# Performance work log

Measured on AMD Instinct MI355X. Metric: run time of the kernel, lower is better.

The kernel has to match this reference:

```python
import jax, jax.numpy as jnp
import numpy as np

B, L, N_IN, N_STATE = 32, 4096, 8, 8
C_IN, C_OUT = N_IN + N_STATE, N_STATE
H, M, N_LAYERS = 64, 64, 4


def setup_inputs() -> dict:
    key = jax.random.key(0)
    ks = jax.random.split(key, 16)
    s = 0.02
    return {
        "u": jax.random.normal(ks[0], (B, L, N_IN), jnp.float32),
        "z": jax.random.normal(ks[1], (B, N_STATE), jnp.float32),
        "t": jax.random.uniform(ks[2], (B, 1), jnp.float32),
        "w_lift": jax.random.normal(ks[3], (H, C_IN), jnp.float32) * s,
        "b_lift": jnp.zeros((H,), jnp.float32),
        "spec_wr": jax.random.normal(ks[4], (N_LAYERS, H, H, M), jnp.float32) / (H),
        "spec_wi": jax.random.normal(ks[5], (N_LAYERS, H, H, M), jnp.float32) / (H),
        "w_skip": jax.random.normal(ks[6], (N_LAYERS, H, H), jnp.float32) * s,
        "b_skip": jnp.zeros((N_LAYERS, H), jnp.float32),
        "w_p1": jax.random.normal(ks[7], (2 * H, H), jnp.float32) * s,
        "b_p1": jnp.zeros((2 * H,), jnp.float32),
        "w_p2": jax.random.normal(ks[8], (C_OUT, 2 * H), jnp.float32) * s,
        "b_p2": jnp.zeros((C_OUT,), jnp.float32),
    }


def _fno_forward(u, z, w_lift, b_lift, spec_wr, spec_wi, w_skip, b_skip, w_p1, b_p1, w_p2, b_p2):
    b, l, _ = u.shape
    rep_z = jnp.broadcast_to(z[:, None, :], (b, l, z.shape[1]))
    x = jnp.concatenate([u, rep_z], axis=-1)          # [B, L, C_in]
    x = jnp.transpose(x, (0, 2, 1))                   # [B, C_in, L]
    # lifting (1x1 conv)
    x = jnp.einsum("bcl,hc->bhl", x, w_lift) + b_lift[None, :, None]
    n_layers, _, _, m = spec_wr.shape
    for i in range(n_layers):
        xf = jnp.fft.rfft(x, axis=-1)                 # [B, H, L//2+1] complex
        w = spec_wr[i] + 1j * spec_wi[i]              # [H, H, M]
        of = jnp.einsum("bim,oim->bom", xf[..., :m], w)
        of = jnp.pad(of, ((0, 0), (0, 0), (0, xf.shape[-1] - m)))
        xs = jnp.fft.irfft(of, n=l, axis=-1)          # [B, H, L]
        sk = jnp.einsum("bil,oi->bol", x, w_skip[i]) + b_skip[i][None, :, None]
        x = xs + sk
        if i < n_layers - 1:
            x = jax.nn.gelu(x)
    # projection: H -> 2H -> C_out (1x1 convs)
    x = jax.nn.gelu(jnp.einsum("bhl,ph->bpl", x, w_p1) + b_p1[None, :, None])
    x = jnp.einsum("bpl,op->bol", x, w_p2) + b_p2[None, :, None]
    outs = jnp.transpose(x, (0, 2, 1))                # [B, L, C_out]
    return outs[:, -1, :]                             # [B, C_out]


def reference(u, z, t, w_lift, b_lift, spec_wr, spec_wi, w_skip, b_skip, w_p1, b_p1, w_p2, b_p2):
    # t is accepted by the original forward but unused in FNOProjection
    return _fno_forward(u, z, w_lift, b_lift, spec_wr, spec_wi, w_skip, b_skip, w_p1, b_p1, w_p2, b_p2)
```

## Files before the change

### kernel.cpp

```cpp
#include <hip/hip_runtime.h>
#include <math.h>

typedef _Float16 f16;
typedef f16  f16x2 __attribute__((ext_vector_type(2)));
typedef f16  f16x4 __attribute__((ext_vector_type(4)));
typedef f16  f16x8 __attribute__((ext_vector_type(8)));
typedef float f32x4 __attribute__((ext_vector_type(4)));

#define F4(p)  (*(float4*)(p))
#define CF4(p) (*(const float4*)(p))

namespace {
constexpr int LL = 4096;
constexpr int HH = 64;
constexpr int NCH = 16;

__device__ __forceinline__ float gelu_fast(float x) {
    float inner = 0.7978845608028654f * (x + 0.044715f * x * x * x);
    float e = __expf(-2.0f * inner);
    return x / (1.0f + e);
}

__device__ __forceinline__ f32x4 mfma16(f16x8 a, f16x8 b, f32x4 c) {
    return __builtin_amdgcn_mfma_f32_16x16x32_f16(a, b, c, 0, 0, 0);
}
}

__global__ __launch_bounds__(256) void k_init(const float* __restrict__ u,
                                              const float* __restrict__ z,
                                              const float* __restrict__ wl,
                                              const float* __restrict__ bl,
                                              const float* __restrict__ wsk,
                                              const float* __restrict__ wr,
                                              const float* __restrict__ wi,
                                              f16* __restrict__ Tdt,
                                              f16* __restrict__ Ttr,
                                              f16* __restrict__ wskh,
                                              f16* __restrict__ wrh,
                                              f16* __restrict__ wih,
                                              f16* __restrict__ XT0) {
    const int bid = blockIdx.x;
    const int t = threadIdx.x;
    if (bid < 512) {
        const int b = bid >> 4;
        const int l0 = (bid & 15) * 256;
        constexpr int IP = 260;
        __shared__ float in_s[16 * IP];
        __shared__ float wsh[64 * 16];
        __shared__ float bsh[64];
        for (int i = t; i < 1024; i += 256) wsh[i] = wl[i];
        if (t < 64) bsh[t] = bl[t];
#pragma unroll
        for (int q = 0; q < 2; ++q) {
            int f = t + q * 256;
            int l = f >> 1, cq = (f & 1) * 4;
            float4 v = CF4(u + ((size_t)b * LL + l0 + l) * 8 + cq);
            in_s[(cq + 0) * IP + l] = v.x;
            in_s[(cq + 1) * IP + l] = v.y;
            in_s[(cq + 2) * IP + l] = v.z;
            in_s[(cq + 3) * IP + l] = v.w;
        }
        for (int f = t; f < 8 * 256; f += 256) {
            int c = f >> 8, l = f & 255;
            in_s[(8 + c) * IP + l] = z[b * 8 + c];
        }
        __syncthreads();
        const int hg = t >> 5, lsub = t & 31;
        float acc[8][8] = {};
        for (int c = 0; c < 16; ++c) {
            float wv[8], inv[8];
#pragma unroll
            for (int i = 0; i < 8; ++i) wv[i] = wsh[(hg * 8 + i) * 16 + c];
#pragma unroll
            for (int j = 0; j < 8; ++j) inv[j] = in_s[c * IP + lsub + 32 * j];
#pragma unroll
            for (int i = 0; i < 8; ++i)
#pragma unroll
                for (int j = 0; j < 8; ++j) acc[i][j] += wv[i] * inv[j];
        }
#pragma unroll
        for (int j = 0; j < 8; ++j) {
            __attribute__((aligned(16))) f16 hv[8];
#pragma unroll
            for (int i = 0; i < 8; ++i) hv[i] = (f16)(acc[i][j] + bsh[hg * 8 + i]);
            int l = l0 + lsub + 32 * j;
            F4(XT0 + ((size_t)b * LL + l) * HH + hg * 8) = CF4(hv);
        }
    } else if (bid < 1536) {
        const int tb = bid - 512;
        const float w0 = 6.283185307179586f / 4096.0f;
        {
            int m = tb >> 4;
            int l = ((tb & 15) << 8) + t;
            float s, c;
            sincosf((float)((l * m) & 4095) * w0, &s, &c);
            Tdt[(size_t)(2 * m) * LL + l]     = (f16)c;
            Tdt[(size_t)(2 * m + 1) * LL + l] = (f16)(-s);
        }
        {
            int l = tb * 4 + (t >> 6);
            int m = t & 63;
            float s, c;
            sincosf((float)((l * m) & 4095) * w0, &s, &c);
            const float sc = 1.0f / 4096.0f;
            f16x2 pv;
            pv.x = (f16)((m == 0) ? sc : 2.0f * sc * c);
            pv.y = (f16)((m == 0) ? 0.0f : -2.0f * sc * s);
            *(f16x2*)(Ttr + (size_t)l * 128 + 2 * m) = pv;
        }
        if (tb < 64) {
            int idx = tb * 256 + t;
            wskh[idx] = (f16)wsk[idx];
        }
    } else {
        const int cb = bid - 1536;
        size_t base = (size_t)cb * 1024 + t * 4;
        float4 vr = CF4(wr + base);
        float4 vi = CF4(wi + base);
        f16x4 hr, hi;
        hr.x = (f16)vr.x; hr.y = (f16)vr.y; hr.z = (f16)vr.z; hr.w = (f16)vr.w;
        hi.x = (f16)vi.x; hi.y = (f16)vi.y; hi.z = (f16)vi.z; hi.w = (f16)vi.w;
        *(f16x4*)(wrh + base) = hr;
        *(f16x4*)(wih + base) = hi;
    }
}

__global__ __launch_bounds__(256) void k_dft(const f16* __restrict__ XT,
                                             const f16* __restrict__ Tdt,
                                             f16* __restrict__ Y) {
    __shared__ f16 Asl[32 * 72];
    __shared__ f16 Bsl[128 * 72];
    const int t = threadIdx.x;
    const int ch = blockIdx.x >> 1, h0 = (blockIdx.x & 1) * 32, b = blockIdx.y;
    const int lane = t & 63, wid = t >> 6;
    const int mh = (wid & 1) * 16, n0 = (wid >> 1) * 64;
    const int fm = lane & 15, fq = lane >> 4;
    const int seg = t >> 6;
    const int br = t >> 3, bcol = (t & 7) * 8;
    f32x4 acc[4] = {};
    f16x8 rA;
    float4 rb[4];
    auto ldAB = [&](int k0) {
        const int l0 = ch * 256 + k0;
        rA = *(const f16x8*)(XT + ((size_t)b * LL + l0 + lane) * HH + h0 + seg * 8);
#pragma unroll
        for (int p = 0; p < 4; ++p)
            rb[p] = CF4(Tdt + (size_t)(br + p * 32) * LL + l0 + bcol);
    };
    auto wrAB = [&]() {
#pragma unroll
        for (int i = 0; i < 8; ++i) Asl[(seg * 8 + i) * 72 + lane] = rA[i];
#pragma unroll
        for (int p = 0; p < 4; ++p)
            F4(&Bsl[(br + p * 32) * 72 + bcol]) = rb[p];
    };
    ldAB(0);
    wrAB();
    for (int k0 = 0; k0 < 256; k0 += 64) {
        if (k0 < 192) ldAB(k0 + 64);
        __syncthreads();
#pragma unroll
        for (int ks = 0; ks < 64; ks += 32) {
            f16x8 a = *(const f16x8*)&Asl[(mh + fm) * 72 + ks + fq * 8];
#pragma unroll
            for (int j = 0; j < 4; ++j) {
                f16x8 bj = *(const f16x8*)&Bsl[(n0 + j * 16 + fm) * 72 + ks + fq * 8];
                acc[j] = mfma16(a, bj, acc[j]);
            }
        }
        __syncthreads();
        if (k0 < 192) wrAB();
    }
    f16* yp = Y + ((size_t)ch * 2048 + b * HH + h0) * 128;
#pragma unroll
    for (int j = 0; j < 4; ++j)
#pragma unroll
        for (int r = 0; r < 4; ++r)
            yp[(size_t)(mh + fq * 4 + r) * 128 + n0 + j * 16 + fm] = (f16)acc[j][r];
}

__global__ __launch_bounds__(256) void k_spec(const f16* __restrict__ Y,
                                              const f16* __restrict__ wrh,
                                              const f16* __restrict__ wih,
                                              f16* __restrict__ Ofh, int layer) {
    __shared__ float xsh[64 * 128];
    const int t = threadIdx.x;
    const int b = blockIdx.x;
    const int og = blockIdx.y;
    {
#pragma unroll
        for (int i = 0; i < 4; ++i) {
            int g = t + i * 256;
            float s[8] = {};
#pragma unroll
            for (int c = 0; c < NCH; ++c) {
                f16x8 v = *(const f16x8*)(Y + ((size_t)c * 2048 + b * HH) * 128 + g * 8);
#pragma unroll
                for (int e = 0; e < 8; ++e) s[e] += (float)v[e];
            }
#pragma unroll
            for (int e = 0; e < 8; ++e) xsh[g * 8 + e] = s[e];
        }
    }
    __syncthreads();
    const int m = t & 63, osub = t >> 6;
    const int o = og * 4 + osub;
    const f16* wrp = wrh + ((size_t)layer * HH + o) * HH * 64 + m;
    const f16* wip = wih + ((size_t)layer * HH + o) * HH * 64 + m;
    float are = 0.0f, aim = 0.0f;
    const float2* xs2 = (const float2*)xsh;
#pragma unroll 8
    for (int i = 0; i < 64; ++i) {
        float2 xv = xs2[i * 64 + m];
        float wrv = (float)wrp[(size_t)i * 64];
        float wiv = (float)wip[(size_t)i * 64];
        are += xv.x * wrv - xv.y * wiv;
        aim += xv.x * wiv + xv.y * wrv;
    }
    f16x2 ov; ov.x = (f16)are; ov.y = (f16)aim;
    *(f16x2*)(Ofh + ((size_t)b * HH + o) * 128 + 2 * m) = ov;
}

__global__ __launch_bounds__(512, 4) void k_fused(const f16* __restrict__ Ofh,
                                                  const f16* __restrict__ XTold,
                                                  const f16* __restrict__ Ttr,
                                                  const f16* __restrict__ wskh,
                                                  const float* __restrict__ bsk,
                                                  const f16* __restrict__ Tdt,
                                                  f16* __restrict__ XTn,
                                                  f16* __restrict__ Y,
                                                  int layer) {
    __shared__ f16 XA[64 * 136];
    __shared__ f16 Asl[64 * 200];
    __shared__ f16 Bsl[128 * 72];
    __shared__ float bss[64];
    const int t = threadIdx.x;
    const int lc = blockIdx.x, b = blockIdx.y;
    const int lane = t & 63, wid = t >> 6;
    const int ow = (wid & 1) * 32;
    const int n0 = (wid >> 1) * 32;
    const int fm = lane & 15, fq = lane >> 4;
    const int br = t >> 3, bcol = (t & 7) * 8;
    {
        int seg = t & 15, row = t >> 4;
#pragma unroll
        for (int p = 0; p < 2; ++p) {
            int r = row + p * 32;
            F4(&Asl[r * 200 + seg * 8]) = CF4(Ofh + ((size_t)(b * HH + r)) * 128 + seg * 8);
        }
        F4(&Asl[br * 200 + 128 + bcol]) =
            CF4(wskh + ((size_t)(layer * HH + br)) * HH + bcol);
        if (t < 64) bss[t] = bsk[layer * HH + t];
    }
    float4 rB0, rB1;
    auto ldR = [&](int ls, int c) {
        const int l0g = lc * 256 + ls * 128;
        if (c < 2) {
            rB0 = CF4(Ttr + (size_t)(l0g + br) * 128 + c * 64 + bcol);
            rB1 = CF4(Ttr + (size_t)(l0g + br + 64) * 128 + c * 64 + bcol);
        } else {
            rB0 = CF4(XTold + ((size_t)b * LL + l0g + br) * HH + bcol);
            rB1 = CF4(XTold + ((size_t)b * LL + l0g + br + 64) * HH + bcol);
        }
    };
    auto ldD = [&](int ls, int c) {
        const int l0 = lc * 256 + ls * 128 + c * 64;
        rB0 = CF4(Tdt + (size_t)br * LL + l0 + bcol);
        rB1 = CF4(Tdt + (size_t)(br + 64) * LL + l0 + bcol);
    };
    auto wrB = [&]() {
        F4(&Bsl[br * 72 + bcol]) = rB0;
        F4(&Bsl[(br + 64) * 72 + bcol]) = rB1;
    };
    f32x4 acc[2][2];
    f32x4 Yac[2][2] = {};
    auto reconMM = [&](int c) {
#pragma unroll
        for (int ks = 0; ks < 64; ks += 32) {
            f16x8 a0 = *(const f16x8*)&Asl[(ow + fm) * 200 + c * 64 + ks + fq * 8];
            f16x8 a1 = *(const f16x8*)&Asl[(ow + 16 + fm) * 200 + c * 64 + ks + fq * 8];
#pragma unroll
            for (int j = 0; j < 2; ++j) {
                f16x8 bj = *(const f16x8*)&Bsl[(n0 + j * 16 + fm) * 72 + ks + fq * 8];
                acc[0][j] = mfma16(a0, bj, acc[0][j]);
                acc[1][j] = mfma16(a1, bj, acc[1][j]);
            }
        }
    };
    auto dftMM = [&](int c) {
#pragma unroll
        for (int ks = 0; ks < 64; ks += 32) {
            f16x8 a0 = *(const f16x8*)&XA[(ow + fm) * 136 + c * 64 + ks + fq * 8];
            f16x8 a1 = *(const f16x8*)&XA[(ow + 16 + fm) * 136 + c * 64 + ks + fq * 8];
#pragma unroll
            for (int j = 0; j < 2; ++j) {
                f16x8 bj = *(const f16x8*)&Bsl[(n0 + j * 16 + fm) * 72 + ks + fq * 8];
                Yac[0][j] = mfma16(a0, bj, Yac[0][j]);
                Yac[1][j] = mfma16(a1, bj, Yac[1][j]);
            }
        }
    };
    ldR(0, 0);
    __syncthreads();
    wrB();
    __syncthreads();
    for (int ls = 0; ls < 2; ++ls) {
        const int l0g = lc * 256 + ls * 128;
#pragma unroll
        for (int i = 0; i < 2; ++i)
#pragma unroll
            for (int j = 0; j < 2; ++j) acc[i][j] = (f32x4){0.f, 0.f, 0.f, 0.f};
        ldR(ls, 1);
        reconMM(0);
        __syncthreads();
        wrB();
        __syncthreads();
        ldR(ls, 2);
        reconMM(1);
        __syncthreads();
        wrB();
        __syncthreads();
        ldD(ls, 0);
        reconMM(2);
        __syncthreads();
#pragma unroll
        for (int i = 0; i < 2; ++i)
#pragma unroll
            for (int r = 0; r < 4; ++r) {
                int row = ow + i * 16 + fq * 4 + r;
                float bias = bss[row];
#pragma unroll
                for (int j = 0; j < 2; ++j) {
                    int lcn = n0 + j * 16 + fm;
                    f16 hv = (f16)gelu_fast(acc[i][j][r] + bias);
                    XA[row * 136 + lcn] = hv;
                    Bsl[lcn * 72 + row] = hv;
                }
            }
        __syncthreads();
        if (layer < 2) {
            F4(XTn + ((size_t)b * LL + l0g + br) * HH + bcol) = CF4(&Bsl[br * 72 + bcol]);
            F4(XTn + ((size_t)b * LL + l0g + br + 64) * HH + bcol) =
                CF4(&Bsl[(br + 64) * 72 + bcol]);
        } else if (lc == NCH - 1 && ls == 1) {
            if (t < 64) XTn[((size_t)b * LL + (LL - 1)) * HH + t] = Bsl[127 * 72 + t];
        }
        __syncthreads();
        wrB();
        __syncthreads();
        ldD(ls, 1);
        dftMM(0);
        __syncthreads();
        wrB();
        __syncthreads();
        if (ls == 0) ldR(1, 0);
        dftMM(1);
        if (ls == 0) {
            __syncthreads();
            wrB();
            __syncthreads();
        }
    }
    f16* yp = Y + ((size_t)lc * 2048 + (size_t)b * HH) * 128;
#pragma unroll
    for (int i = 0; i < 2; ++i)
#pragma unroll
        for (int j = 0; j < 2; ++j)
#pragma unroll
            for (int r = 0; r < 4; ++r)
                yp[(size_t)(ow + i * 16 + fq * 4 + r) * 128 + n0 + j * 16 + fm] =
                    (f16)Yac[i][j][r];
}

__global__ __launch_bounds__(128) void k_final(const f16* __restrict__ Ofh,
                                               const f16* __restrict__ XT3,
                                               const f16* __restrict__ Ttr,
                                               const float* __restrict__ wsk,
                                               const float* __restrict__ bsk,
                                               const float* __restrict__ wp1,
                                               const float* __restrict__ bp1,
                                               const float* __restrict__ wp2,
                                               const float* __restrict__ bp2,
                                               float* __restrict__ out) {
    __shared__ float ofs[64 * 129];
    __shared__ float wsks[64 * 65];
    __shared__ float wp1s[128 * 65];
    __shared__ float tl[128], xl[64], x4[64], y[128];
    const int b = blockIdx.x, t = threadIdx.x;
    {
#pragma unroll
        for (int i = 0; i < 8; ++i) {
            int g = t + i * 128;
            f16x8 v = *(const f16x8*)(Ofh + (size_t)b * HH * 128 + g * 8);
            int o = g >> 4, k0 = (g & 15) * 8;
#pragma unroll
            for (int e = 0; e < 8; ++e) ofs[o * 129 + k0 + e] = (float)v[e];
        }
    }
    {
        const float* src = wsk + 3 * HH * HH;
#pragma unroll
        for (int i = 0; i < 8; ++i) {
            int g = t + i * 128;
            float4 v = CF4(src + g * 4);
            int o = g >> 4, c0 = (g & 15) * 4;
            F4(&wsks[o * 65 + c0]) = v;
        }
    }
    {
#pragma unroll
        for (int i = 0; i < 16; ++i) {
            int g = t + i * 128;
            float4 v = CF4(wp1 + g * 4);
            int p = g >> 4, c0 = (g & 15) * 4;
            F4(&wp1s[p * 65 + c0]) = v;
        }
    }
    tl[t] = (float)Ttr[(size_t)(LL - 1) * 128 + t];
    if (t < 64) xl[t] = (float)XT3[((size_t)b * LL + (LL - 1)) * HH + t];
    __syncthreads();
    if (t < 64) {
        const int o = t;
        float acc = bsk[3 * HH + o];
        for (int k = 0; k < 128; ++k) acc += ofs[o * 129 + k] * tl[k];
        for (int i = 0; i < 64; ++i) acc += wsks[o * 65 + i] * xl[i];
        x4[o] = acc;
    }
    __syncthreads();
    {
        float acc = bp1[t];
        for (int h = 0; h < 64; ++h) acc += wp1s[t * 65 + h] * x4[h];
        y[t] = gelu_fast(acc);
    }
    __syncthreads();
    if (t < 8) {
        float acc = bp2[t];
        for (int p = 0; p < 128; ++p) acc += wp2[t * 128 + p] * y[p];
        out[b * 8 + t] = acc;
    }
}

extern "C" void kernel_launch(void* const* d_in, const int* in_sizes, int n_in,
                              void* d_out, int out_size, void* d_ws, size_t ws_size,
                              hipStream_t stream) {
    (void)in_sizes; (void)n_in; (void)out_size; (void)ws_size;
    const float* u   = (const float*)d_in[0];
    const float* z   = (const float*)d_in[1];
    const float* wl  = (const float*)d_in[3];
    const float* bl  = (const float*)d_in[4];
    const float* swr = (const float*)d_in[5];
    const float* swi = (const float*)d_in[6];
    const float* wsk = (const float*)d_in[7];
    const float* bsk = (const float*)d_in[8];
    const float* wp1 = (const float*)d_in[9];
    const float* bp1 = (const float*)d_in[10];
    const float* wp2 = (const float*)d_in[11];
    const float* bp2 = (const float*)d_in[12];
    float* out = (float*)d_out;

    f16* ws    = (f16*)d_ws;
    f16* XTa   = ws;
    f16* XTb   = XTa + 8388608;
    f16* Tdt   = XTb + 8388608;
    f16* Ttr   = Tdt + 524288;
    f16* Ofh   = Ttr + 524288;
    f16* wskh  = Ofh + 262144;
    f16* wrh   = wskh + 16384;
    f16* wih   = wrh + 1048576;
    f16* Yb    = wih + 1048576;

    k_init<<<2560, 256, 0, stream>>>(u, z, wl, bl, wsk, swr, swi,
                                     Tdt, Ttr, wskh, wrh, wih, XTa);

    k_dft<<<dim3(32, 32), 256, 0, stream>>>(XTa, Tdt, Yb);

    f16* xtc = XTa; f16* xtn = XTb;
    for (int layer = 0; layer < 4; ++layer) {
        k_spec<<<dim3(32, 16), 256, 0, stream>>>(Yb, wrh, wih, Ofh, layer);
        if (layer < 3) {
            k_fused<<<dim3(16, 32), 512, 0, stream>>>(Ofh, xtc, Ttr, wskh, bsk,
                                                      Tdt, xtn, Yb, layer);
            f16* tmp = xtc; xtc = xtn; xtn = tmp;
        } else {
            k_final<<<32, 128, 0, stream>>>(Ofh, xtc, Ttr, wsk, bsk,
                                            wp1, bp1, wp2, bp2, out);
        }
    }
}
```

Before: 217.5 us.

## Double-buffer B tiles in fused kernel and simplify DFT tile loading

In the fused layer kernel, a single B staging buffer becomes two ping-pong buffers in one manually laid-out shared-memory block. Each next tile can then be written while the current one is consumed, which removes about half of the __syncthreads barriers per stage. The cost is roughly 18 KB more LDS per block, which may limit how many blocks fit on a CU. The DFT kernel separately drops its register-prefetch pipeline in favour of direct global-to-LDS loads bracketed by barriers, trading latency hiding for fewer live registers.

```diff
diff --git a/kernel.cpp b/kernel.cpp
--- a/kernel.cpp
+++ b/kernel.cpp
@@ -135,29 +135,21 @@
     const int lane = t & 63, wid = t >> 6;
     const int mh = (wid & 1) * 16, n0 = (wid >> 1) * 64;
     const int fm = lane & 15, fq = lane >> 4;
-    const int seg = t >> 6;
-    const int br = t >> 3, bcol = (t & 7) * 8;
     f32x4 acc[4] = {};
-    f16x8 rA;
-    float4 rb[4];
-    auto ldAB = [&](int k0) {
+    for (int k0 = 0; k0 < 256; k0 += 64) {
         const int l0 = ch * 256 + k0;
-        rA = *(const f16x8*)(XT + ((size_t)b * LL + l0 + lane) * HH + h0 + seg * 8);
-#pragma unroll
-        for (int p = 0; p < 4; ++p)
-            rb[p] = CF4(Tdt + (size_t)(br + p * 32) * LL + l0 + bcol);
-    };
-    auto wrAB = [&]() {
-#pragma unroll
-        for (int i = 0; i < 8; ++i) Asl[(seg * 8 + i) * 72 + lane] = rA[i];
-#pragma unroll
-        for (int p = 0; p < 4; ++p)
-            F4(&Bsl[(br + p * 32) * 72 + bcol]) = rb[p];
-    };
-    ldAB(0);
-    wrAB();
-    for (int k0 = 0; k0 < 256; k0 += 64) {
-        if (k0 < 192) ldAB(k0 + 64);
+        __syncthreads();
+        {
+            int seg = t >> 6;
+            f16x8 v = *(const f16x8*)(XT + ((size_t)b * LL + l0 + lane) * HH + h0 + seg * 8);
+#pragma unroll
+            for (int i = 0; i < 8; ++i) Asl[(seg * 8 + i) * 72 + lane] = v[i];
+        }
+#pragma unroll
+        for (int p = 0; p < 4; ++p) {
+            int r = (t >> 3) + p * 32;
+            F4(&Bsl[r * 72 + (t & 7) * 8]) = CF4(Tdt + (size_t)r * LL + l0 + (t & 7) * 8);
+        }
         __syncthreads();
 #pragma unroll
         for (int ks = 0; ks < 64; ks += 32) {
@@ -168,8 +160,6 @@
                 acc[j] = mfma16(a, bj, acc[j]);
             }
         }
-        __syncthreads();
-        if (k0 < 192) wrAB();
     }
     f16* yp = Y + ((size_t)ch * 2048 + b * HH + h0) * 128;
 #pragma unroll
@@ -230,10 +220,12 @@
                                                   f16* __restrict__ XTn,
                                                   f16* __restrict__ Y,
                                                   int layer) {
-    __shared__ f16 XA[64 * 136];
-    __shared__ f16 Asl[64 * 200];
-    __shared__ f16 Bsl[128 * 72];
-    __shared__ float bss[64];
+    __shared__ __align__(16) char smem[80128];
+    f16* Asl = (f16*)smem;
+    f16* XA  = (f16*)(smem + 25600);
+    f16* B0  = (f16*)(smem + 43008);
+    f16* B1  = (f16*)(smem + 61440);
+    float* bss = (float*)(smem + 79872);
     const int t = threadIdx.x;
     const int lc = blockIdx.x, b = blockIdx.y;
     const int lane = t & 63, wid = t >> 6;
@@ -241,17 +233,7 @@
     const int n0 = (wid >> 1) * 32;
     const int fm = lane & 15, fq = lane >> 4;
     const int br = t >> 3, bcol = (t & 7) * 8;
-    {
-        int seg = t & 15, row = t >> 4;
-#pragma unroll
-        for (int p = 0; p < 2; ++p) {
-            int r = row + p * 32;
-            F4(&Asl[r * 200 + seg * 8]) = CF4(Ofh + ((size_t)(b * HH + r)) * 128 + seg * 8);
-        }
-        F4(&Asl[br * 200 + 128 + bcol]) =
-            CF4(wskh + ((size_t)(layer * HH + br)) * HH + bcol);
-        if (t < 64) bss[t] = bsk[layer * HH + t];
-    }
+
     float4 rB0, rB1;
     auto ldR = [&](int ls, int c) {
         const int l0g = lc * 256 + ls * 128;
@@ -268,60 +250,74 @@
         rB0 = CF4(Tdt + (size_t)br * LL + l0 + bcol);
         rB1 = CF4(Tdt + (size_t)(br + 64) * LL + l0 + bcol);
     };
-    auto wrB = [&]() {
-        F4(&Bsl[br * 72 + bcol]) = rB0;
-        F4(&Bsl[(br + 64) * 72 + bcol]) = rB1;
+    auto wrB = [&](f16* buf) {
+        F4(&buf[br * 72 + bcol]) = rB0;
+        F4(&buf[(br + 64) * 72 + bcol]) = rB1;
     };
     f32x4 acc[2][2];
     f32x4 Yac[2][2] = {};
-    auto reconMM = [&](int c) {
+    auto reconMM = [&](const f16* buf, int k0) {
 #pragma unroll
         for (int ks = 0; ks < 64; ks += 32) {
-            f16x8 a0 = *(const f16x8*)&Asl[(ow + fm) * 200 + c * 64 + ks + fq * 8];
-            f16x8 a1 = *(const f16x8*)&Asl[(ow + 16 + fm) * 200 + c * 64 + ks + fq * 8];
+            f16x8 a0 = *(const f16x8*)&Asl[(ow + fm) * 200 + k0 + ks + fq * 8];
+            f16x8 a1 = *(const f16x8*)&Asl[(ow + 16 + fm) * 200 + k0 + ks + fq * 8];
 #pragma unroll
             for (int j = 0; j < 2; ++j) {
-                f16x8 bj = *(const f16x8*)&Bsl[(n0 + j * 16 + fm) * 72 + ks + fq * 8];
+                f16x8 bj = *(const f16x8*)&buf[(n0 + j * 16 + fm) * 72 + ks + fq * 8];
                 acc[0][j] = mfma16(a0, bj, acc[0][j]);
                 acc[1][j] = mfma16(a1, bj, acc[1][j]);
             }
         }
     };
-    auto dftMM = [&](int c) {
+    auto dftMM = [&](const f16* buf, int c) {
 #pragma unroll
         for (int ks = 0; ks < 64; ks += 32) {
             f16x8 a0 = *(const f16x8*)&XA[(ow + fm) * 136 + c * 64 + ks + fq * 8];
             f16x8 a1 = *(const f16x8*)&XA[(ow + 16 + fm) * 136 + c * 64 + ks + fq * 8];
 #pragma unroll
             for (int j = 0; j < 2; ++j) {
-                f16x8 bj = *(const f16x8*)&Bsl[(n0 + j * 16 + fm) * 72 + ks + fq * 8];
+                f16x8 bj = *(const f16x8*)&buf[(n0 + j * 16 + fm) * 72 + ks + fq * 8];
                 Yac[0][j] = mfma16(a0, bj, Yac[0][j]);
                 Yac[1][j] = mfma16(a1, bj, Yac[1][j]);
             }
         }
     };
-    ldR(0, 0);
+
+    {
+        int seg = t & 15, row = t >> 4;
+#pragma unroll
+        for (int p = 0; p < 2; ++p) {
+            int r = row + p * 32;
+            F4(&Asl[r * 200 + seg * 8]) = CF4(Ofh + ((size_t)(b * HH + r)) * 128 + seg * 8);
+        }
+        F4(&Asl[br * 200 + 128 + bcol]) =
+            CF4(wskh + ((size_t)(layer * HH + br)) * HH + bcol);
+        if (t < 64) bss[t] = bsk[layer * HH + t];
+        ldR(0, 0);
+        wrB(B0);
+    }
     __syncthreads();
-    wrB();
-    __syncthreads();
+
+#pragma unroll
     for (int ls = 0; ls < 2; ++ls) {
         const int l0g = lc * 256 + ls * 128;
+        f16* bA = (ls == 0) ? B0 : B1;
+        f16* bB = (ls == 0) ? B1 : B0;
 #pragma unroll
         for (int i = 0; i < 2; ++i)
 #pragma unroll
             for (int j = 0; j < 2; ++j) acc[i][j] = (f32x4){0.f, 0.f, 0.f, 0.f};
         ldR(ls, 1);
-        reconMM(0);
-        __syncthreads();
-        wrB();
+        reconMM(bA, 0);
+        wrB(bB);
         __syncthreads();
         ldR(ls, 2);
-        reconMM(1);
-        __syncthreads();
-        wrB();
+        reconMM(bB, 64);
+        wrB(bA);
         __syncthreads();
         ldD(ls, 0);
-        reconMM(2);
+        reconMM(bA, 128);
+        wrB(bB);
         __syncthreads();
 #pragma unroll
         for (int i = 0; i < 2; ++i)
@@ -334,32 +330,26 @@
                     int lcn = n0 + j * 16 + fm;
                     f16 hv = (f16)gelu_fast(acc[i][j][r] + bias);
                     XA[row * 136 + lcn] = hv;
-                    Bsl[lcn * 72 + row] = hv;
+                    bA[lcn * 72 + row] = hv;
                 }
             }
         __syncthreads();
         if (layer < 2) {
-            F4(XTn + ((size_t)b * LL + l0g + br) * HH + bcol) = CF4(&Bsl[br * 72 + bcol]);
+            F4(XTn + ((size_t)b * LL + l0g + br) * HH + bcol) = CF4(&bA[br * 72 + bcol]);
             F4(XTn + ((size_t)b * LL + l0g + br + 64) * HH + bcol) =
-                CF4(&Bsl[(br + 64) * 72 + bcol]);
+                CF4(&bA[(br + 64) * 72 + bcol]);
         } else if (lc == NCH - 1 && ls == 1) {
-            if (t < 64) XTn[((size_t)b * LL + (LL - 1)) * HH + t] = Bsl[127 * 72 + t];
-        }
-        __syncthreads();
-        wrB();
-        __syncthreads();
+            if (t < 64) XTn[((size_t)b * LL + (LL - 1)) * HH + t] = bA[127 * 72 + t];
+        }
         ldD(ls, 1);
-        dftMM(0);
-        __syncthreads();
-        wrB();
-        __syncthreads();
+        dftMM(bB, 0);
+        __syncthreads();
+        wrB(bA);
         if (ls == 0) ldR(1, 0);
-        dftMM(1);
-        if (ls == 0) {
-            __syncthreads();
-            wrB();
-            __syncthreads();
-        }
+        __syncthreads();
+        dftMM(bA, 1);
+        if (ls == 0) wrB(bB);
+        __syncthreads();
     }
     f16* yp = Y + ((size_t)lc * 2048 + (size_t)b * HH) * 128;
 #pragma unroll
```

Result: faster. 199.7 us (-8.2%).
